# Optimization experiments

Measured on AMD Instinct MI355X. Metric: run time of the kernel, lower is better.

## Reference

```python
import jax, jax.numpy as jnp
import numpy as np

B, S, E = 8, 4096, 256
NQ, F = 8, 1024


def setup_inputs() -> dict:
    key = jax.random.key(0)
    k1, k2, k3, k4 = jax.random.split(key, 4)
    x = jax.random.normal(k1, (B, S, E), dtype=jnp.float32)
    theta = jax.random.normal(k2, (NQ,), dtype=jnp.float32)
    W1 = jax.random.normal(k3, (F, NQ), dtype=jnp.float32) * (1.0 / np.sqrt(NQ))
    W2 = jax.random.normal(k4, (E, F), dtype=jnp.float32) * (1.0 / np.sqrt(F))
    return {"x": x, "theta": theta, "W1": W1, "W2": W2}


def reference(x, theta, W1, W2):
    # Quantum layer: per wire w, |0> -> RX(x_w) -> RY(theta_w) -> <Z>.
    # No entangling gates => product state; exact closed form:
    #   <Z_w> = cos(x_w) * cos(theta_w)
    nq = theta.shape[0]
    q = jnp.cos(x[..., :nq]) * jnp.cos(theta)           # [B, S, nq]
    # dropout is identity in eval mode (p interpreted at inference)
    h = jax.nn.relu(jnp.einsum('bsq,fq->bsf', q, W1))   # [B, S, F]
    return jnp.einsum('bsf,ef->bse', h, W2)             # [B, S, E]
```

## Files before the change

kernel.cpp:

```cpp
#include <hip/hip_runtime.h>
#include <hip/hip_bf16.h>

typedef __attribute__((ext_vector_type(8))) short  short8_t;
typedef __attribute__((ext_vector_type(4))) float  float4_t;
typedef __attribute__((ext_vector_type(4))) int    int4_t;
typedef __attribute__((ext_vector_type(2))) unsigned int uint2_t;

#define BM 64
#define BN 128
#define BK 64
#define HSTR 72

__device__ __forceinline__ unsigned short f2bf(float f) {
    unsigned int u = __builtin_bit_cast(unsigned int, f);
    u += 0x7FFFu + ((u >> 16) & 1u);
    return (unsigned short)(u >> 16);
}
__device__ __forceinline__ unsigned int pack2(float a, float b) {
    return (unsigned int)f2bf(a) | ((unsigned int)f2bf(b) << 16);
}
__device__ __forceinline__ void gload_lds16(const void* g, void* l) {
    __builtin_amdgcn_global_load_lds(
        (const __attribute__((address_space(1))) void*)g,
        (__attribute__((address_space(3))) void*)l, 16, 0, 0);
}

__global__ void cvt_kernel(const float* __restrict__ src, unsigned short* __restrict__ dst) {
    const int i = (blockIdx.x * blockDim.x + threadIdx.x) * 4;
    const float4_t v = *reinterpret_cast<const float4_t*>(src + i);
    unsigned long long p = (unsigned long long)pack2(v[0], v[1])
                         | ((unsigned long long)pack2(v[2], v[3]) << 32);
    *reinterpret_cast<unsigned long long*>(dst + i) = p;
}

template <bool WSOK>
__global__ __launch_bounds__(256, 4)
void ffq_kernel(const float* __restrict__ x,
                const float* __restrict__ theta,
                const float* __restrict__ W1f,
                const unsigned short* __restrict__ W1b,
                const float* __restrict__ W2f,
                const unsigned short* __restrict__ W2b,
                float* __restrict__ out)
{
    __shared__ __align__(16) unsigned short qs[BM][8];
    __shared__ __align__(16) unsigned short hs[BM][HSTR];
    __shared__ __align__(16) unsigned short Bs[BN][BK];

    const int tid  = threadIdx.x;
    const int lane = tid & 63;
    const int w    = tid >> 6;
    const int bid  = blockIdx.x;
    const int rowbase = (bid >> 1) * BM;
    const int colbase = (bid & 1) * BN;

    if (w == 0) {
        const float* xp = x + (size_t)(rowbase + lane) * 256;
        const float4_t x0 = *reinterpret_cast<const float4_t*>(xp);
        const float4_t x1 = *reinterpret_cast<const float4_t*>(xp + 4);
        float qv[8];
        #pragma unroll
        for (int j = 0; j < 4; ++j) {
            qv[j]     = __cosf(x0[j]) * __cosf(theta[j]);
            qv[4 + j] = __cosf(x1[j]) * __cosf(theta[4 + j]);
        }
        int4_t pq;
        pq[0] = (int)pack2(qv[0], qv[1]);
        pq[1] = (int)pack2(qv[2], qv[3]);
        pq[2] = (int)pack2(qv[4], qv[5]);
        pq[3] = (int)pack2(qv[6], qv[7]);
        *reinterpret_cast<int4_t*>(&qs[lane][0]) = pq;
    }
    __syncthreads();

    short8_t qf[4];
    #pragma unroll
    for (int mt = 0; mt < 4; ++mt) {
        short8_t v = {0, 0, 0, 0, 0, 0, 0, 0};
        if (lane < 16) v = *reinterpret_cast<const short8_t*>(&qs[mt * 16 + lane][0]);
        qf[mt] = v;
    }

    float4_t acc[2][4];
    #pragma unroll
    for (int i = 0; i < 2; ++i)
        #pragma unroll
        for (int j = 0; j < 4; ++j)
            acc[i][j] = (float4_t){0.f, 0.f, 0.f, 0.f};

    const int lr  = lane & 15;
    const int lkg = lane >> 4;
    const int lk  = lkg * 8;
    const int er  = lane >> 3;
    const int js  = lane & 7;

    for (int kc = 0; kc < 1024; kc += BK) {
        __syncthreads();

        #pragma unroll
        for (int it = 0; it < 4; ++it) {
            const int e = w * 32 + it * 8 + er;
            const int srccol = ((js ^ (e & 7)) << 3);
            if constexpr (WSOK) {
                const unsigned short* src = W2b + (size_t)(colbase + e) * 1024 + kc + srccol;
                gload_lds16(src, &Bs[w * 32 + it * 8][0]);
            } else {
                const float* src = W2f + (size_t)(colbase + e) * 1024 + kc + srccol;
                const float4_t v0 = *reinterpret_cast<const float4_t*>(src);
                const float4_t v1 = *reinterpret_cast<const float4_t*>(src + 4);
                int4_t p;
                p[0] = (int)pack2(v0[0], v0[1]);
                p[1] = (int)pack2(v0[2], v0[3]);
                p[2] = (int)pack2(v1[0], v1[1]);
                p[3] = (int)pack2(v1[2], v1[3]);
                *reinterpret_cast<int4_t*>(&Bs[e][js * 8]) = p;
            }
        }

        short8_t af = {0, 0, 0, 0, 0, 0, 0, 0};
        if (lane < 16) {
            if constexpr (WSOK) {
                af = *reinterpret_cast<const short8_t*>(W1b + (size_t)(kc + w * 16 + lane) * 8);
            } else {
                const float* src = W1f + (size_t)(kc + w * 16 + lane) * 8;
                const float4_t v0 = *reinterpret_cast<const float4_t*>(src);
                const float4_t v1 = *reinterpret_cast<const float4_t*>(src + 4);
                int4_t p;
                p[0] = (int)pack2(v0[0], v0[1]);
                p[1] = (int)pack2(v0[2], v0[3]);
                p[2] = (int)pack2(v1[0], v1[1]);
                p[3] = (int)pack2(v1[2], v1[3]);
                af = __builtin_bit_cast(short8_t, p);
            }
        }

        #pragma unroll
        for (int mt = 0; mt < 4; ++mt) {
            float4_t d = __builtin_amdgcn_mfma_f32_16x16x32_bf16(
                af, qf[mt], (float4_t){0.f, 0.f, 0.f, 0.f}, 0, 0, 0);
            uint2_t pk;
            pk[0] = pack2(fmaxf(d[0], 0.f), fmaxf(d[1], 0.f));
            pk[1] = pack2(fmaxf(d[2], 0.f), fmaxf(d[3], 0.f));
            *reinterpret_cast<uint2_t*>(&hs[mt * 16 + lr][w * 16 + lkg * 4]) = pk;
        }

        __syncthreads();

        const int wr = w >> 1, wc = w & 1;
        #pragma unroll
        for (int kk = 0; kk < BK; kk += 32) {
            const short8_t a0 = *reinterpret_cast<const short8_t*>(
                &hs[wr * 32 + 0  + lr][kk + lk]);
            const short8_t a1 = *reinterpret_cast<const short8_t*>(
                &hs[wr * 32 + 16 + lr][kk + lk]);
            const int s = (kk + lk) >> 3;
            #pragma unroll
            for (int cf = 0; cf < 4; ++cf) {
                const int e = wc * 64 + cf * 16 + lr;
                const short8_t b = *reinterpret_cast<const short8_t*>(
                    &Bs[e][(s ^ (e & 7)) << 3]);
                acc[0][cf] = __builtin_amdgcn_mfma_f32_16x16x32_bf16(a0, b, acc[0][cf], 0, 0, 0);
                acc[1][cf] = __builtin_amdgcn_mfma_f32_16x16x32_bf16(a1, b, acc[1][cf], 0, 0, 0);
            }
        }
    }

    const int wr = w >> 1, wc = w & 1;
    const int lq = lane >> 4;
    #pragma unroll
    for (int rf = 0; rf < 2; ++rf) {
        #pragma unroll
        for (int cf = 0; cf < 4; ++cf) {
            #pragma unroll
            for (int r = 0; r < 4; ++r) {
                const int gr = rowbase + wr * 32 + rf * 16 + lq * 4 + r;
                const int gc = colbase + wc * 64 + cf * 16 + lr;
                out[(size_t)gr * 256 + gc] = acc[rf][cf][r];
            }
        }
    }
}

extern "C" void kernel_launch(void* const* d_in, const int* in_sizes, int n_in,
                              void* d_out, int out_size, void* d_ws, size_t ws_size,
                              hipStream_t stream) {
    const float* x     = (const float*)d_in[0];
    const float* theta = (const float*)d_in[1];
    const float* W1    = (const float*)d_in[2];
    const float* W2    = (const float*)d_in[3];
    float* out = (float*)d_out;

    const size_t need = (size_t)(256 * 1024 + 8 * 1024) * sizeof(unsigned short);
    const bool wsok = (ws_size >= need);

    if (wsok) {
        unsigned short* W2b = (unsigned short*)d_ws;
        unsigned short* W1b = W2b + 256 * 1024;
        cvt_kernel<<<256, 256, 0, stream>>>(W2, W2b);
        cvt_kernel<<<8,   256, 0, stream>>>(W1, W1b);
        ffq_kernel<true><<<1024, 256, 0, stream>>>(x, theta, nullptr, W1b, nullptr, W2b, out);
    } else {
        ffq_kernel<false><<<1024, 256, 0, stream>>>(x, theta, W1, nullptr, W2, nullptr, out);
    }
}
```

Before: 41.89 us.

## Double-buffer W2 tile and hidden activations to overlap loads with MFMA

Splits the shared W2 tile and the hidden-activation buffer into two halves. The next chunk's W2 global-to-LDS load and W1 fragment load are issued right after the barrier, so they run while the current chunk's MFMAs execute, and the next hidden tile is computed into registers after those MFMAs. This drops one barrier per iteration and is meant to hide global-load latency. In exchange it doubles LDS use and lowers the launch-bounds occupancy hint from 4 to 3 blocks per CU.

```diff
diff --git a/kernel.cpp b/kernel.cpp
--- a/kernel.cpp
+++ b/kernel.cpp
@@ -10,6 +10,7 @@
 #define BN 128
 #define BK 64
 #define HSTR 72
+#define NCHUNK 16
 
 __device__ __forceinline__ unsigned short f2bf(float f) {
     unsigned int u = __builtin_bit_cast(unsigned int, f);
@@ -34,7 +35,7 @@
 }
 
 template <bool WSOK>
-__global__ __launch_bounds__(256, 4)
+__global__ __launch_bounds__(256, 3)
 void ffq_kernel(const float* __restrict__ x,
                 const float* __restrict__ theta,
                 const float* __restrict__ W1f,
@@ -44,8 +45,8 @@
                 float* __restrict__ out)
 {
     __shared__ __align__(16) unsigned short qs[BM][8];
-    __shared__ __align__(16) unsigned short hs[BM][HSTR];
-    __shared__ __align__(16) unsigned short Bs[BN][BK];
+    __shared__ __align__(16) unsigned short hs[2][BM][HSTR];
+    __shared__ __align__(16) unsigned short Bs[2][BN][BK];
 
     const int tid  = threadIdx.x;
     const int lane = tid & 63;
@@ -93,17 +94,16 @@
     const int lk  = lkg * 8;
     const int er  = lane >> 3;
     const int js  = lane & 7;
-
-    for (int kc = 0; kc < 1024; kc += BK) {
-        __syncthreads();
-
+    const int wr  = w >> 1, wc = w & 1;
+
+    auto stage = [&](int buf, int kc) {
         #pragma unroll
         for (int it = 0; it < 4; ++it) {
             const int e = w * 32 + it * 8 + er;
             const int srccol = ((js ^ (e & 7)) << 3);
             if constexpr (WSOK) {
-                const unsigned short* src = W2b + (size_t)(colbase + e) * 1024 + kc + srccol;
-                gload_lds16(src, &Bs[w * 32 + it * 8][0]);
+                gload_lds16(W2b + (size_t)(colbase + e) * 1024 + kc + srccol,
+                            &Bs[buf][w * 32 + it * 8][0]);
             } else {
                 const float* src = W2f + (size_t)(colbase + e) * 1024 + kc + srccol;
                 const float4_t v0 = *reinterpret_cast<const float4_t*>(src);
@@ -113,10 +113,12 @@
                 p[1] = (int)pack2(v0[2], v0[3]);
                 p[2] = (int)pack2(v1[0], v1[1]);
                 p[3] = (int)pack2(v1[2], v1[3]);
-                *reinterpret_cast<int4_t*>(&Bs[e][js * 8]) = p;
-            }
-        }
-
+                *reinterpret_cast<int4_t*>(&Bs[buf][e][js * 8]) = p;
+            }
+        }
+    };
+
+    auto load_af = [&](int kc) -> short8_t {
         short8_t af = {0, 0, 0, 0, 0, 0, 0, 0};
         if (lane < 16) {
             if constexpr (WSOK) {
@@ -133,39 +135,58 @@
                 af = __builtin_bit_cast(short8_t, p);
             }
         }
-
+        return af;
+    };
+
+    uint2_t pk[4];
+    auto hcompute = [&](short8_t af) {
         #pragma unroll
         for (int mt = 0; mt < 4; ++mt) {
             float4_t d = __builtin_amdgcn_mfma_f32_16x16x32_bf16(
                 af, qf[mt], (float4_t){0.f, 0.f, 0.f, 0.f}, 0, 0, 0);
-            uint2_t pk;
-            pk[0] = pack2(fmaxf(d[0], 0.f), fmaxf(d[1], 0.f));
-            pk[1] = pack2(fmaxf(d[2], 0.f), fmaxf(d[3], 0.f));
-            *reinterpret_cast<uint2_t*>(&hs[mt * 16 + lr][w * 16 + lkg * 4]) = pk;
-        }
+            pk[mt][0] = pack2(fmaxf(d[0], 0.f), fmaxf(d[1], 0.f));
+            pk[mt][1] = pack2(fmaxf(d[2], 0.f), fmaxf(d[3], 0.f));
+        }
+    };
+
+    stage(0, 0);
+    hcompute(load_af(0));
+
+    for (int k = 0; k < NCHUNK; ++k) {
+        const int cur = k & 1, nxt = cur ^ 1;
+
+        #pragma unroll
+        for (int mt = 0; mt < 4; ++mt)
+            *reinterpret_cast<uint2_t*>(&hs[cur][mt * 16 + lr][w * 16 + lkg * 4]) = pk[mt];
 
         __syncthreads();
 
-        const int wr = w >> 1, wc = w & 1;
+        short8_t afn;
+        if (k + 1 < NCHUNK) {
+            stage(nxt, (k + 1) * BK);
+            afn = load_af((k + 1) * BK);
+        }
+
         #pragma unroll
         for (int kk = 0; kk < BK; kk += 32) {
             const short8_t a0 = *reinterpret_cast<const short8_t*>(
-                &hs[wr * 32 + 0  + lr][kk + lk]);
+                &hs[cur][wr * 32 + 0  + lr][kk + lk]);
             const short8_t a1 = *reinterpret_cast<const short8_t*>(
-                &hs[wr * 32 + 16 + lr][kk + lk]);
+                &hs[cur][wr * 32 + 16 + lr][kk + lk]);
             const int s = (kk + lk) >> 3;
             #pragma unroll
             for (int cf = 0; cf < 4; ++cf) {
                 const int e = wc * 64 + cf * 16 + lr;
                 const short8_t b = *reinterpret_cast<const short8_t*>(
-                    &Bs[e][(s ^ (e & 7)) << 3]);
+                    &Bs[cur][e][(s ^ (e & 7)) << 3]);
                 acc[0][cf] = __builtin_amdgcn_mfma_f32_16x16x32_bf16(a0, b, acc[0][cf], 0, 0, 0);
                 acc[1][cf] = __builtin_amdgcn_mfma_f32_16x16x32_bf16(a1, b, acc[1][cf], 0, 0, 0);
             }
         }
-    }
-
-    const int wr = w >> 1, wc = w & 1;
+
+        if (k + 1 < NCHUNK) hcompute(afn);
+    }
+
     const int lq = lane >> 4;
     #pragma unroll
     for (int rf = 0; rf < 2; ++rf) {
```

Measured after the change: 43.76 us. 4.5% more time.

## Keep hidden activations in registers via permlane swaps, drop LDS and barriers

Applied to the files above, without the earlier changes.

Each wave now owns an independent 64x64 output tile. It recomputes the first-layer MFMA outputs and turns them into A-operand fragments in registers using v_permlane32/16 swaps, instead of staging h through shared memory with block barriers. W2 is pre-converted by a single fused prep kernel into a k-sliced bf16 layout so each lane can load B fragments straight from global/L2 without LDS staging. The cost is that W2 traffic is no longer shared across waves, the first-layer work is recomputed per column tile (4x), register pressure is higher (launch bounds 2), and the grid is halved.

```diff
diff --git a/kernel.cpp b/kernel.cpp
--- a/kernel.cpp
+++ b/kernel.cpp
@@ -6,179 +6,188 @@
 typedef __attribute__((ext_vector_type(4))) int    int4_t;
 typedef __attribute__((ext_vector_type(2))) unsigned int uint2_t;
 
-#define BM 64
-#define BN 128
-#define BK 64
-#define HSTR 72
-
 __device__ __forceinline__ unsigned short f2bf(float f) {
     unsigned int u = __builtin_bit_cast(unsigned int, f);
     u += 0x7FFFu + ((u >> 16) & 1u);
     return (unsigned short)(u >> 16);
 }
-__device__ __forceinline__ unsigned int pack2(float a, float b) {
+__device__ __forceinline__ unsigned int cvtpk(float a, float b) {
     return (unsigned int)f2bf(a) | ((unsigned int)f2bf(b) << 16);
 }
-__device__ __forceinline__ void gload_lds16(const void* g, void* l) {
-    __builtin_amdgcn_global_load_lds(
-        (const __attribute__((address_space(1))) void*)g,
-        (__attribute__((address_space(3))) void*)l, 16, 0, 0);
-}
-
-__global__ void cvt_kernel(const float* __restrict__ src, unsigned short* __restrict__ dst) {
-    const int i = (blockIdx.x * blockDim.x + threadIdx.x) * 4;
-    const float4_t v = *reinterpret_cast<const float4_t*>(src + i);
-    unsigned long long p = (unsigned long long)pack2(v[0], v[1])
-                         | ((unsigned long long)pack2(v[2], v[3]) << 32);
-    *reinterpret_cast<unsigned long long*>(dst + i) = p;
+__device__ __forceinline__ void plane32_swap(unsigned int& a, unsigned int& b) {
+    asm volatile("v_permlane32_swap_b32 %0, %1" : "+v"(a), "+v"(b));
+}
+__device__ __forceinline__ void plane16_swap(unsigned int& a, unsigned int& b) {
+    asm volatile("v_permlane16_swap_b32 %0, %1" : "+v"(a), "+v"(b));
+}
+
+__global__ void prep_kernel(const float* __restrict__ W2, const float* __restrict__ W1,
+                            unsigned short* __restrict__ W2s, unsigned short* __restrict__ W1b) {
+    const int bid = blockIdx.x, tid = threadIdx.x;
+    if (bid < 128) {
+        const int idx = bid * 256 + tid;
+        const int e   = idx >> 7;
+        const int ks  = idx & 127;
+        const float* src = W2 + (size_t)e * 1024 + ks * 8;
+        const float4_t v0 = *reinterpret_cast<const float4_t*>(src);
+        const float4_t v1 = *reinterpret_cast<const float4_t*>(src + 4);
+        int4_t p;
+        p[0] = (int)cvtpk(v0[0], v0[1]);
+        p[1] = (int)cvtpk(v0[2], v0[3]);
+        p[2] = (int)cvtpk(v1[0], v1[1]);
+        p[3] = (int)cvtpk(v1[2], v1[3]);
+        *reinterpret_cast<int4_t*>(W2s + ((size_t)ks * 256 + e) * 8) = p;
+    } else {
+        const int base = tid * 32;
+        #pragma unroll
+        for (int it = 0; it < 8; ++it) {
+            const float4_t v = *reinterpret_cast<const float4_t*>(W1 + base + it * 4);
+            uint2_t p;
+            p[0] = cvtpk(v[0], v[1]);
+            p[1] = cvtpk(v[2], v[3]);
+            *reinterpret_cast<uint2_t*>(W1b + base + it * 4) = p;
+        }
+    }
 }
 
 template <bool WSOK>
-__global__ __launch_bounds__(256, 4)
+__global__ __launch_bounds__(256, 2)
 void ffq_kernel(const float* __restrict__ x,
                 const float* __restrict__ theta,
                 const float* __restrict__ W1f,
                 const unsigned short* __restrict__ W1b,
                 const float* __restrict__ W2f,
-                const unsigned short* __restrict__ W2b,
+                const unsigned short* __restrict__ W2s,
                 float* __restrict__ out)
 {
-    __shared__ __align__(16) unsigned short qs[BM][8];
-    __shared__ __align__(16) unsigned short hs[BM][HSTR];
-    __shared__ __align__(16) unsigned short Bs[BN][BK];
-
     const int tid  = threadIdx.x;
     const int lane = tid & 63;
     const int w    = tid >> 6;
     const int bid  = blockIdx.x;
-    const int rowbase = (bid >> 1) * BM;
-    const int colbase = (bid & 1) * BN;
-
-    if (w == 0) {
-        const float* xp = x + (size_t)(rowbase + lane) * 256;
-        const float4_t x0 = *reinterpret_cast<const float4_t*>(xp);
-        const float4_t x1 = *reinterpret_cast<const float4_t*>(xp + 4);
-        float qv[8];
-        #pragma unroll
-        for (int j = 0; j < 4; ++j) {
-            qv[j]     = __cosf(x0[j]) * __cosf(theta[j]);
-            qv[4 + j] = __cosf(x1[j]) * __cosf(theta[4 + j]);
-        }
-        int4_t pq;
-        pq[0] = (int)pack2(qv[0], qv[1]);
-        pq[1] = (int)pack2(qv[2], qv[3]);
-        pq[2] = (int)pack2(qv[4], qv[5]);
-        pq[3] = (int)pack2(qv[6], qv[7]);
-        *reinterpret_cast<int4_t*>(&qs[lane][0]) = pq;
-    }
-    __syncthreads();
+    const int ntile = bid & 3;
+    const int mtile = (bid >> 2) * 4 + w;
+    const int rowbase = mtile * 64;
+    const int colbase = ntile * 64;
+    const int lr = lane & 15;
+    const int G  = lane >> 4;
+
+    float th[8];
+    #pragma unroll
+    for (int j = 0; j < 8; ++j) th[j] = theta[j];
 
     short8_t qf[4];
     #pragma unroll
     for (int mt = 0; mt < 4; ++mt) {
         short8_t v = {0, 0, 0, 0, 0, 0, 0, 0};
-        if (lane < 16) v = *reinterpret_cast<const short8_t*>(&qs[mt * 16 + lane][0]);
+        if (lane < 16) {
+            const float* xp = x + (size_t)(rowbase + mt * 16 + lane) * 256;
+            const float4_t x0 = *reinterpret_cast<const float4_t*>(xp);
+            const float4_t x1 = *reinterpret_cast<const float4_t*>(xp + 4);
+            float qv[8];
+            #pragma unroll
+            for (int j = 0; j < 4; ++j) {
+                qv[j]     = __cosf(x0[j]) * __cosf(th[j]);
+                qv[4 + j] = __cosf(x1[j]) * __cosf(th[4 + j]);
+            }
+            int4_t pq;
+            pq[0] = (int)cvtpk(qv[0], qv[1]);
+            pq[1] = (int)cvtpk(qv[2], qv[3]);
+            pq[2] = (int)cvtpk(qv[4], qv[5]);
+            pq[3] = (int)cvtpk(qv[6], qv[7]);
+            v = __builtin_bit_cast(short8_t, pq);
+        }
         qf[mt] = v;
     }
 
-    float4_t acc[2][4];
-    #pragma unroll
-    for (int i = 0; i < 2; ++i)
+    float4_t acc[4][4];
+    #pragma unroll
+    for (int i = 0; i < 4; ++i)
         #pragma unroll
         for (int j = 0; j < 4; ++j)
             acc[i][j] = (float4_t){0.f, 0.f, 0.f, 0.f};
 
-    const int lr  = lane & 15;
-    const int lkg = lane >> 4;
-    const int lk  = lkg * 8;
-    const int er  = lane >> 3;
-    const int js  = lane & 7;
-
-    for (int kc = 0; kc < 1024; kc += BK) {
-        __syncthreads();
-
-        #pragma unroll
-        for (int it = 0; it < 4; ++it) {
-            const int e = w * 32 + it * 8 + er;
-            const int srccol = ((js ^ (e & 7)) << 3);
-            if constexpr (WSOK) {
-                const unsigned short* src = W2b + (size_t)(colbase + e) * 1024 + kc + srccol;
-                gload_lds16(src, &Bs[w * 32 + it * 8][0]);
-            } else {
-                const float* src = W2f + (size_t)(colbase + e) * 1024 + kc + srccol;
-                const float4_t v0 = *reinterpret_cast<const float4_t*>(src);
-                const float4_t v1 = *reinterpret_cast<const float4_t*>(src + 4);
-                int4_t p;
-                p[0] = (int)pack2(v0[0], v0[1]);
-                p[1] = (int)pack2(v0[2], v0[3]);
-                p[2] = (int)pack2(v1[0], v1[1]);
-                p[3] = (int)pack2(v1[2], v1[3]);
-                *reinterpret_cast<int4_t*>(&Bs[e][js * 8]) = p;
-            }
-        }
-
-        short8_t af = {0, 0, 0, 0, 0, 0, 0, 0};
+    for (int kc = 0; kc < 1024; kc += 32) {
+        short8_t af0 = {0, 0, 0, 0, 0, 0, 0, 0};
+        short8_t af1 = {0, 0, 0, 0, 0, 0, 0, 0};
         if (lane < 16) {
             if constexpr (WSOK) {
-                af = *reinterpret_cast<const short8_t*>(W1b + (size_t)(kc + w * 16 + lane) * 8);
+                af0 = *reinterpret_cast<const short8_t*>(W1b + (size_t)(kc + lane) * 8);
+                af1 = *reinterpret_cast<const short8_t*>(W1b + (size_t)(kc + 16 + lane) * 8);
             } else {
-                const float* src = W1f + (size_t)(kc + w * 16 + lane) * 8;
-                const float4_t v0 = *reinterpret_cast<const float4_t*>(src);
-                const float4_t v1 = *reinterpret_cast<const float4_t*>(src + 4);
-                int4_t p;
-                p[0] = (int)pack2(v0[0], v0[1]);
-                p[1] = (int)pack2(v0[2], v0[3]);
-                p[2] = (int)pack2(v1[0], v1[1]);
-                p[3] = (int)pack2(v1[2], v1[3]);
-                af = __builtin_bit_cast(short8_t, p);
-            }
-        }
-
+                #pragma unroll
+                for (int t = 0; t < 2; ++t) {
+                    const float* src = W1f + (size_t)(kc + t * 16 + lane) * 8;
+                    const float4_t v0 = *reinterpret_cast<const float4_t*>(src);
+                    const float4_t v1 = *reinterpret_cast<const float4_t*>(src + 4);
+                    int4_t p;
+                    p[0] = (int)cvtpk(v0[0], v0[1]);
+                    p[1] = (int)cvtpk(v0[2], v0[3]);
+                    p[2] = (int)cvtpk(v1[0], v1[1]);
+                    p[3] = (int)cvtpk(v1[2], v1[3]);
+                    if (t == 0) af0 = __builtin_bit_cast(short8_t, p);
+                    else        af1 = __builtin_bit_cast(short8_t, p);
+                }
+            }
+        }
+
+        short8_t bf[4];
+        #pragma unroll
+        for (int cf = 0; cf < 4; ++cf) {
+            const int e = colbase + cf * 16 + lr;
+            if constexpr (WSOK) {
+                bf[cf] = *reinterpret_cast<const short8_t*>(
+                    W2s + (((size_t)(kc >> 3) + G) * 256 + e) * 8);
+            } else {
+                const float* p = W2f + (size_t)e * 1024 + kc + G * 8;
+                const float4_t v0 = *reinterpret_cast<const float4_t*>(p);
+                const float4_t v1 = *reinterpret_cast<const float4_t*>(p + 4);
+                int4_t pb;
+                pb[0] = (int)cvtpk(v0[0], v0[1]);
+                pb[1] = (int)cvtpk(v0[2], v0[3]);
+                pb[2] = (int)cvtpk(v1[0], v1[1]);
+                pb[3] = (int)cvtpk(v1[2], v1[3]);
+                bf[cf] = __builtin_bit_cast(short8_t, pb);
+            }
+        }
+
+        short8_t afrag[4];
         #pragma unroll
         for (int mt = 0; mt < 4; ++mt) {
-            float4_t d = __builtin_amdgcn_mfma_f32_16x16x32_bf16(
-                af, qf[mt], (float4_t){0.f, 0.f, 0.f, 0.f}, 0, 0, 0);
-            uint2_t pk;
-            pk[0] = pack2(fmaxf(d[0], 0.f), fmaxf(d[1], 0.f));
-            pk[1] = pack2(fmaxf(d[2], 0.f), fmaxf(d[3], 0.f));
-            *reinterpret_cast<uint2_t*>(&hs[mt * 16 + lr][w * 16 + lkg * 4]) = pk;
-        }
-
-        __syncthreads();
-
-        const int wr = w >> 1, wc = w & 1;
-        #pragma unroll
-        for (int kk = 0; kk < BK; kk += 32) {
-            const short8_t a0 = *reinterpret_cast<const short8_t*>(
-                &hs[wr * 32 + 0  + lr][kk + lk]);
-            const short8_t a1 = *reinterpret_cast<const short8_t*>(
-                &hs[wr * 32 + 16 + lr][kk + lk]);
-            const int s = (kk + lk) >> 3;
+            const float4_t t0 = __builtin_amdgcn_mfma_f32_16x16x32_bf16(
+                af0, qf[mt], (float4_t){0.f, 0.f, 0.f, 0.f}, 0, 0, 0);
+            const float4_t t1 = __builtin_amdgcn_mfma_f32_16x16x32_bf16(
+                af1, qf[mt], (float4_t){0.f, 0.f, 0.f, 0.f}, 0, 0, 0);
+            unsigned int A_ = cvtpk(fmaxf(t0[0], 0.f), fmaxf(t0[1], 0.f));
+            unsigned int B_ = cvtpk(fmaxf(t0[2], 0.f), fmaxf(t0[3], 0.f));
+            unsigned int C_ = cvtpk(fmaxf(t1[0], 0.f), fmaxf(t1[1], 0.f));
+            unsigned int D_ = cvtpk(fmaxf(t1[2], 0.f), fmaxf(t1[3], 0.f));
+            plane32_swap(A_, C_);
+            plane16_swap(A_, C_);
+            plane32_swap(B_, D_);
+            plane16_swap(B_, D_);
+            int4_t ua;
+            ua[0] = (int)A_; ua[1] = (int)B_; ua[2] = (int)C_; ua[3] = (int)D_;
+            afrag[mt] = __builtin_bit_cast(short8_t, ua);
+        }
+
+        #pragma unroll
+        for (int mt = 0; mt < 4; ++mt)
             #pragma unroll
-            for (int cf = 0; cf < 4; ++cf) {
-                const int e = wc * 64 + cf * 16 + lr;
-                const short8_t b = *reinterpret_cast<const short8_t*>(
-                    &Bs[e][(s ^ (e & 7)) << 3]);
-                acc[0][cf] = __builtin_amdgcn_mfma_f32_16x16x32_bf16(a0, b, acc[0][cf], 0, 0, 0);
-                acc[1][cf] = __builtin_amdgcn_mfma_f32_16x16x32_bf16(a1, b, acc[1][cf], 0, 0, 0);
-            }
-        }
-    }
-
-    const int wr = w >> 1, wc = w & 1;
-    const int lq = lane >> 4;
-    #pragma unroll
-    for (int rf = 0; rf < 2; ++rf) {
-        #pragma unroll
-        for (int cf = 0; cf < 4; ++cf) {
+            for (int cf = 0; cf < 4; ++cf)
+                acc[mt][cf] = __builtin_amdgcn_mfma_f32_16x16x32_bf16(
+                    afrag[mt], bf[cf], acc[mt][cf], 0, 0, 0);
+    }
+
+    #pragma unroll
+    for (int mt = 0; mt < 4; ++mt)
+        #pragma unroll
+        for (int cf = 0; cf < 4; ++cf)
             #pragma unroll
             for (int r = 0; r < 4; ++r) {
-                const int gr = rowbase + wr * 32 + rf * 16 + lq * 4 + r;
-                const int gc = colbase + wc * 64 + cf * 16 + lr;
-                out[(size_t)gr * 256 + gc] = acc[rf][cf][r];
-            }
-        }
-    }
+                const int gr = rowbase + mt * 16 + G * 4 + r;
+                const int gc = colbase + cf * 16 + lr;
+                out[(size_t)gr * 256 + gc] = acc[mt][cf][r];
+            }
 }
 
 extern "C" void kernel_launch(void* const* d_in, const int* in_sizes, int n_in,
@@ -194,12 +203,11 @@
     const bool wsok = (ws_size >= need);
 
     if (wsok) {
-        unsigned short* W2b = (unsigned short*)d_ws;
-        unsigned short* W1b = W2b + 256 * 1024;
-        cvt_kernel<<<256, 256, 0, stream>>>(W2, W2b);
-        cvt_kernel<<<8,   256, 0, stream>>>(W1, W1b);
-        ffq_kernel<true><<<1024, 256, 0, stream>>>(x, theta, nullptr, W1b, nullptr, W2b, out);
+        unsigned short* W2s = (unsigned short*)d_ws;
+        unsigned short* W1b = W2s + 256 * 1024;
+        prep_kernel<<<129, 256, 0, stream>>>(W2, W1, W2s, W1b);
+        ffq_kernel<true><<<512, 256, 0, stream>>>(x, theta, nullptr, W1b, nullptr, W2s, out);
     } else {
-        ffq_kernel<false><<<1024, 256, 0, stream>>>(x, theta, W1, nullptr, W2, nullptr, out);
-    }
-}
+        ffq_kernel<false><<<512, 256, 0, stream>>>(x, theta, W1, nullptr, W2, nullptr, out);
+    }
+}
```

Measured after the change: 51.41 us. 1.23x slower.
